# Kernel tuning notes

Measured on AMD Instinct MI355X. Metric: run time of the kernel, lower is better.

## Reference

```python
import jax, jax.numpy as jnp
import numpy as np

POOL_H, POOL_W = 7, 7
SPATIAL_SCALE = 0.25
SAMPLING_RATIO = 2
ALIGNED = True


def setup_inputs() -> dict:
    key = jax.random.key(0)
    k1, k2, k3, k4, k5 = jax.random.split(key, 5)
    N, C, H, W = 4, 256, 200, 200
    K = 1024
    feat = jax.random.normal(k1, (N, C, H, W), dtype=jnp.float32)
    # boxes in image coordinates (image side = H / spatial_scale = 800)
    img = H / SPATIAL_SCALE
    b = jax.random.randint(k2, (K,), 0, N).astype(jnp.float32)
    x1 = jax.random.uniform(k3, (K,)) * (img - 32.0)
    y1 = jax.random.uniform(k4, (K,)) * (img - 32.0)
    wh = jax.random.uniform(k5, (K, 2)) * 256.0 + 16.0
    x2 = jnp.minimum(x1 + wh[:, 0], img - 1.0)
    y2 = jnp.minimum(y1 + wh[:, 1], img - 1.0)
    rois = jnp.stack([b, x1, y1, x2, y2], axis=1)
    return {"input": feat, "rois": rois}


def _roi_align(feat, rois):
    N, C, H, W = feat.shape
    K = rois.shape[0]
    S = SAMPLING_RATIO
    offset = 0.5 if ALIGNED else 0.0

    batch_idx = rois[:, 0].astype(jnp.int32)
    x1 = rois[:, 1] * SPATIAL_SCALE - offset
    y1 = rois[:, 2] * SPATIAL_SCALE - offset
    x2 = rois[:, 3] * SPATIAL_SCALE - offset
    y2 = rois[:, 4] * SPATIAL_SCALE - offset
    roi_w = x2 - x1
    roi_h = y2 - y1
    if not ALIGNED:  # legacy: clamp roi size to at least 1
        roi_w = jnp.maximum(roi_w, 1.0)
        roi_h = jnp.maximum(roi_h, 1.0)
    bin_h = roi_h / POOL_H  # [K]
    bin_w = roi_w / POOL_W

    # sample coordinates: ys [K, PH, S], xs [K, PW, S]
    ph = jnp.arange(POOL_H, dtype=jnp.float32)
    pw = jnp.arange(POOL_W, dtype=jnp.float32)
    s = (jnp.arange(S, dtype=jnp.float32) + 0.5) / S
    ys = y1[:, None, None] + (ph[None, :, None] + s[None, None, :]) * bin_h[:, None, None]
    xs = x1[:, None, None] + (pw[None, :, None] + s[None, None, :]) * bin_w[:, None, None]

    # broadcast to full sample grid [K, PH, S, PW, S]
    y = ys[:, :, :, None, None]
    x = xs[:, None, None, :, :]
    valid = (y > -1.0) & (y < H) & (x > -1.0) & (x < W)

    yc = jnp.clip(y, 0.0, H - 1)
    xc = jnp.clip(x, 0.0, W - 1)
    y0 = jnp.floor(yc).astype(jnp.int32)
    x0 = jnp.floor(xc).astype(jnp.int32)
    y1i = jnp.minimum(y0 + 1, H - 1)
    x1i = jnp.minimum(x0 + 1, W - 1)
    ly = yc - y0
    lx = xc - x0
    hy = 1.0 - ly
    hx = 1.0 - lx

    bi = batch_idx[:, None, None, None, None]
    # advanced indexing -> [K, PH, S, PW, S, C]
    v00 = feat[bi, :, y0, x0]
    v01 = feat[bi, :, y0, x1i]
    v10 = feat[bi, :, y1i, x0]
    v11 = feat[bi, :, y1i, x1i]

    val = ((hy * hx)[..., None] * v00 + (hy * lx)[..., None] * v01
           + (ly * hx)[..., None] * v10 + (ly * lx)[..., None] * v11)
    val = jnp.where(valid[..., None], val, 0.0)

    out = val.sum(axis=(2, 4)) / (S * S)  # [K, PH, PW, C]
    return jnp.transpose(out, (0, 3, 1, 2))  # [K, C, PH, PW]


def reference(input, rois):
    return _roi_align(input, rois)
```

## Files before the change

kernel.cpp:

```cpp
#include <hip/hip_runtime.h>

#define POOL_H 7
#define POOL_W 7
#define BINS   49
#define SR 2
#define SCALE 0.25f
#define CH 256

typedef unsigned int   u32;
typedef unsigned short u16;
typedef unsigned long long u64;
typedef float f2v __attribute__((ext_vector_type(2)));
typedef f2v uf2 __attribute__((aligned(4)));
typedef float f4  __attribute__((ext_vector_type(4)));
typedef u16  us4 __attribute__((ext_vector_type(4)));
typedef u32  ui2 __attribute__((ext_vector_type(2)));
typedef u32  ui4 __attribute__((ext_vector_type(4)));

__device__ __forceinline__ u16 f32_to_bf16_rne(float f) {
    u32 u = __builtin_bit_cast(u32, f);
    u32 r = (u + 0x7FFFu + ((u >> 16) & 1u)) >> 16;
    return (u16)r;
}
__device__ __forceinline__ float bf16lo(u32 u) { return __builtin_bit_cast(float, u << 16); }
__device__ __forceinline__ float bf16hi(u32 u) { return __builtin_bit_cast(float, u & 0xFFFF0000u); }

__global__ __launch_bounds__(512) void nchw_to_nhwc_bf16(
    const float* __restrict__ feat, u16* __restrict__ ft,
    const float* __restrict__ rois, int* __restrict__ perm,
    int HW, int tiles, int K, int H, int W)
{
    __shared__ __align__(16) unsigned char smem[64 * 260 * 2];

    int t = threadIdx.x;

    if ((int)blockIdx.x == gridDim.x - 1) {
        u64* keys = (u64*)smem;
        int bd = (int)blockDim.x;
        for (int v = t; v < 1024; v += bd) {
            u64 kv = ~0ull;
            if (v < K) {
                const float* rp = rois + (size_t)v * 5;
                int b = (int)rp[0];
                float cx = 0.5f * (rp[1] + rp[3]) * SCALE;
                float cy = 0.5f * (rp[2] + rp[4]) * SCALE;
                int qx = min(15, max(0, (int)(cx * (16.0f / (float)W))));
                int qy = min(15, max(0, (int)(cy * (16.0f / (float)H))));
                u32 m = 0;
                #pragma unroll
                for (int i = 0; i < 4; ++i)
                    m |= (((qy >> i) & 1u) << (2 * i + 1)) | (((qx >> i) & 1u) << (2 * i));
                u32 key = ((u32)b << 8) | m;
                kv = ((u64)key << 32) | (u32)v;
            }
            keys[v] = kv;
        }
        __syncthreads();
        for (int size = 2; size <= 1024; size <<= 1) {
            for (int stride = size >> 1; stride > 0; stride >>= 1) {
                for (int v = t; v < 1024; v += bd) {
                    int j = v ^ stride;
                    if (j > v) {
                        bool up = ((v & size) == 0);
                        u64 a = keys[v], bb = keys[j];
                        if ((a > bb) == up) { keys[v] = bb; keys[j] = a; }
                    }
                }
                __syncthreads();
            }
        }
        for (int v = t; v < K; v += bd)
            perm[v] = (int)(keys[v] & 0xffffffffu);
        return;
    }

    u16 (*lds)[260] = (u16 (*)[260])smem;
    int b    = blockIdx.x / tiles;
    int tile = blockIdx.x % tiles;
    int hw0  = tile * 64;

    int lane = t & 63;
    int w    = t >> 6;

    const float* src = feat + (size_t)b * CH * HW + hw0 + lane;
    #pragma unroll 4
    for (int i = 0; i < 32; ++i) {
        int c = w + 8 * i;
        float v = src[(size_t)c * HW];
        lds[lane][c] = f32_to_bf16_rne(v);
    }
    __syncthreads();

    u16* dst = ft + ((size_t)b * HW + hw0) * CH;
    #pragma unroll
    for (int it = 0; it < 4; ++it) {
        int id = it * 512 + t;
        int r  = id >> 5;
        int o  = (id & 31) * 8;
        ui2 lo = __builtin_bit_cast(ui2, *(const us4*)&lds[r][o]);
        ui2 hi = __builtin_bit_cast(ui2, *(const us4*)&lds[r][o + 4]);
        ui4 v = { lo.x, lo.y, hi.x, hi.y };
        *(ui4*)(dst + (size_t)id * 8) = v;
    }
}

__global__ __launch_bounds__(448) void roi_gather_nhwc(
    const u16* __restrict__ ft,
    const float* __restrict__ rois,
    const int* __restrict__ perm,
    float* __restrict__ out,
    int H, int W, int K, int chunk, int do_swz)
{
    int bid  = blockIdx.x;
    int slot = do_swz ? (bid & 7) * chunk + (bid >> 3) : bid;
    int k    = perm[slot / 7];
    int q    = slot % 7;
    int bin0 = q * 7;

    __shared__ float lds[7][CH];

    int lane = threadIdx.x & 63;
    int w    = threadIdx.x >> 6;
    int half = lane >> 5;
    int lc   = lane & 31;

    const float* rp = rois + (size_t)k * 5;
    int   b   = (int)rp[0];
    float rx1 = rp[1] * SCALE - 0.5f;
    float ry1 = rp[2] * SCALE - 0.5f;
    float rx2 = rp[3] * SCALE - 0.5f;
    float ry2 = rp[4] * SCALE - 0.5f;
    float bin_h = (ry2 - ry1) * (1.0f / POOL_H);
    float bin_w = (rx2 - rx1) * (1.0f / POOL_W);

    const u16* fbase = ft + (size_t)b * H * W * CH + lc * 8;

    int ph = q;
    int pw = w;

    float acc[8];
    #pragma unroll
    for (int j = 0; j < 8; ++j) acc[j] = 0.0f;

    #pragma unroll
    for (int iy = 0; iy < SR; ++iy) {
        float y = ry1 + ((float)ph + ((float)iy + 0.5f) * (1.0f / SR)) * bin_h;
        bool vy = (y > -1.0f) && (y < (float)H);
        float yc = fminf(fmaxf(y, 0.0f), (float)(H - 1));
        int   y0 = (int)yc;
        int   y1 = min(y0 + 1, H - 1);
        float ly = yc - (float)y0;
        float hy = 1.0f - ly;
        int   ysel = half ? y1 : y0;
        float wrow = half ? ly : hy;
        #pragma unroll
        for (int ix = 0; ix < SR; ++ix) {
            float x = rx1 + ((float)pw + ((float)ix + 0.5f) * (1.0f / SR)) * bin_w;
            bool vx = (x > -1.0f) && (x < (float)W);
            if (!(vy && vx)) continue;
            float xc = fminf(fmaxf(x, 0.0f), (float)(W - 1));
            int   x0 = (int)xc;
            int   x1 = min(x0 + 1, W - 1);
            float lx = xc - (float)x0;

            const u16* p0 = fbase + (size_t)(ysel * W + x0) * CH;
            ui4 A = *(const ui4*)p0;
            ui4 B = *(const ui4*)(p0 + (size_t)(x1 - x0) * CH);

            #pragma unroll
            for (int j = 0; j < 4; ++j) {
                float a0 = bf16lo(A[j]), a1 = bf16hi(A[j]);
                float b0 = bf16lo(B[j]), b1 = bf16hi(B[j]);
                float r0 = a0 + lx * (b0 - a0);
                float r1 = a1 + lx * (b1 - a1);
                acc[2 * j]     += wrow * r0;
                acc[2 * j + 1] += wrow * r1;
            }
        }
    }

    #pragma unroll
    for (int j = 0; j < 8; ++j)
        acc[j] = (acc[j] + __shfl_xor(acc[j], 32, 64)) * 0.25f;

    if (half == 0) {
        f4 lo = { acc[0], acc[1], acc[2], acc[3] };
        f4 hi = { acc[4], acc[5], acc[6], acc[7] };
        *(f4*)&lds[w][lc * 8]     = lo;
        *(f4*)&lds[w][lc * 8 + 4] = hi;
    }
    __syncthreads();

    float* ob = out + (size_t)k * CH * BINS + bin0;
    for (int id = (int)threadIdx.x; id < 7 * CH; id += 448) {
        int c  = id / 7;
        int lb = id % 7;
        ob[(size_t)c * BINS + lb] = lds[lb][c];
    }
}

#define NC 2
#define NXCD 8
__global__ __launch_bounds__(256) void roi_align_fallback(
    const float* __restrict__ feat, const float* __restrict__ rois,
    float* __restrict__ out, int C, int H, int W, int K,
    int blocks_per_slice, int slices_per_xcd)
{
    int wgid  = blockIdx.x;
    int g     = wgid % NXCD;
    int r     = wgid / NXCD;
    int slice = g * slices_per_xcd + r / blocks_per_slice;
    int j     = r % blocks_per_slice;
    int tid = j * (int)blockDim.x + (int)threadIdx.x;
    int k   = tid / BINS;
    int bin = tid % BINS;
    if (k >= K) return;
    int pw = bin % POOL_W, ph = bin / POOL_W, c2 = slice;

    const float* rp = rois + (size_t)k * 5;
    int b = (int)rp[0];
    float rx1 = rp[1]*SCALE-0.5f, ry1 = rp[2]*SCALE-0.5f;
    float rx2 = rp[3]*SCALE-0.5f, ry2 = rp[4]*SCALE-0.5f;
    float bin_h = (ry2-ry1)*(1.0f/POOL_H), bin_w = (rx2-rx1)*(1.0f/POOL_W);

    int yr0[SR], yr1[SR]; float ly[SR], hy[SR]; bool vy[SR];
    #pragma unroll
    for (int iy = 0; iy < SR; ++iy) {
        float y = ry1 + ((float)ph + ((float)iy+0.5f)*(1.0f/SR))*bin_h;
        vy[iy] = (y > -1.0f) && (y < (float)H);
        float yc = fminf(fmaxf(y, 0.0f), (float)(H-1));
        int y0 = (int)yc; yr0[iy]=y0; yr1[iy]=min(y0+1,H-1);
        ly[iy]=yc-(float)y0; hy[iy]=1.0f-ly[iy];
    }
    int xl[SR]; float lx[SR]; bool vx[SR], xhi[SR];
    #pragma unroll
    for (int ix = 0; ix < SR; ++ix) {
        float x = rx1 + ((float)pw + ((float)ix+0.5f)*(1.0f/SR))*bin_w;
        vx[ix] = (x > -1.0f) && (x < (float)W);
        float xc = fminf(fmaxf(x, 0.0f), (float)(W-1));
        int x0 = (int)xc; int xload = min(x0, W-2);
        xl[ix]=xload; xhi[ix]=(x0>xload); lx[ix]=xc-(float)x0;
    }
    const size_t HW = (size_t)H*W;
    const float* fmap = feat + ((size_t)b*C + (size_t)c2*NC)*HW;
    float acc[NC];
    #pragma unroll
    for (int cc=0; cc<NC; ++cc) acc[cc]=0.0f;
    #pragma unroll
    for (int iy=0; iy<SR; ++iy)
      #pragma unroll
      for (int ix=0; ix<SR; ++ix)
        if (vy[iy] && vx[ix]) {
            int off0 = yr0[iy]*W + xl[ix], off1 = yr1[iy]*W + xl[ix];
            #pragma unroll
            for (int cc=0; cc<NC; ++cc) {
                const float* base = fmap + (size_t)cc*HW;
                f2v d0 = *(const uf2*)(base + off0);
                f2v d1 = *(const uf2*)(base + off1);
                float v00 = xhi[ix] ? d0.y : d0.x;
                float v10 = xhi[ix] ? d1.y : d1.x;
                float r0 = v00 + lx[ix]*(d0.y - v00);
                float r1 = v10 + lx[ix]*(d1.y - v10);
                acc[cc] += hy[iy]*r0 + ly[iy]*r1;
            }
        }
    size_t obase = ((size_t)k*C + (size_t)c2*NC)*BINS + bin;
    #pragma unroll
    for (int cc=0; cc<NC; ++cc)
        out[obase + (size_t)cc*BINS] = acc[cc]*(1.0f/(SR*SR));
}

extern "C" void kernel_launch(void* const* d_in, const int* in_sizes, int n_in,
                              void* d_out, int out_size, void* d_ws, size_t ws_size,
                              hipStream_t stream) {
    const float* feat = (const float*)d_in[0];
    const float* rois = (const float*)d_in[1];
    float* out = (float*)d_out;

    const int C = 256, H = 200, W = 200;
    const int HW = H * W;
    const int K = in_sizes[1] / 5;
    const int N = in_sizes[0] / (C * HW);

    size_t nhwc_bytes = (size_t)N * HW * CH * sizeof(u16);
    size_t need = nhwc_bytes + (size_t)K * sizeof(int);
    if (ws_size >= need && (HW % 64) == 0 && K <= 1024) {
        u16* ft   = (u16*)d_ws;
        int* perm = (int*)((char*)d_ws + nhwc_bytes);
        const int tiles = HW / 64;
        nchw_to_nhwc_bf16<<<N * tiles + 1, 512, 0, stream>>>(
            feat, ft, rois, perm, HW, tiles, K, H, W);
        int grid  = K * 7;
        int swz   = (grid % 8) == 0;
        int chunk = grid / 8;
        roi_gather_nhwc<<<grid, 448, 0, stream>>>(
            (const u16*)ft, rois, perm, out, H, W, K, chunk, swz);
    } else {
        const int threads_per_slice = K * BINS;
        const int block = 256;
        const int blocks_per_slice = (threads_per_slice + block - 1) / block;
        const int slices = C / NC;
        const int slices_per_xcd = slices / NXCD;
        const int grid = slices * blocks_per_slice;
        roi_align_fallback<<<grid, block, 0, stream>>>(feat, rois, out, C, H, W, K,
                                                       blocks_per_slice, slices_per_xcd);
    }
}
```

Before: 92.80 us.

## Widen NCHW-to-NHWC transpose tiles to 128 pixels with packed bf16 pair loads

Measured after the change: 91.86 us. Within noise of the previous version (-1.0%).

```diff
diff --git a/kernel.cpp b/kernel.cpp
--- a/kernel.cpp
+++ b/kernel.cpp
@@ -13,8 +13,6 @@
 typedef float f2v __attribute__((ext_vector_type(2)));
 typedef f2v uf2 __attribute__((aligned(4)));
 typedef float f4  __attribute__((ext_vector_type(4)));
-typedef u16  us4 __attribute__((ext_vector_type(4)));
-typedef u32  ui2 __attribute__((ext_vector_type(2)));
 typedef u32  ui4 __attribute__((ext_vector_type(4)));
 
 __device__ __forceinline__ u16 f32_to_bf16_rne(float f) {
@@ -30,7 +28,7 @@
     const float* __restrict__ rois, int* __restrict__ perm,
     int HW, int tiles, int K, int H, int W)
 {
-    __shared__ __align__(16) unsigned char smem[64 * 260 * 2];
+    extern __shared__ __align__(16) unsigned char smem[];
 
     int t = threadIdx.x;
 
@@ -74,33 +72,58 @@
         return;
     }
 
-    u16 (*lds)[260] = (u16 (*)[260])smem;
+    u32* lds32 = (u32*)smem;
     int b    = blockIdx.x / tiles;
     int tile = blockIdx.x % tiles;
-    int hw0  = tile * 64;
+    int hw0  = tile * 128;
+    int nhw  = min(128, HW - hw0);
 
     int lane = t & 63;
     int w    = t >> 6;
 
-    const float* src = feat + (size_t)b * CH * HW + hw0 + lane;
-    #pragma unroll 4
-    for (int i = 0; i < 32; ++i) {
-        int c = w + 8 * i;
-        float v = src[(size_t)c * HW];
-        lds[lane][c] = f32_to_bf16_rne(v);
+    const float* src = feat + (size_t)b * CH * HW + hw0;
+    if (nhw == 128) {
+        #pragma unroll 8
+        for (int ci = 0; ci < 32; ++ci) {
+            int c = w * 32 + ci;
+            f2v v = *(const f2v*)(src + (size_t)c * HW + 2 * lane);
+            u32 p = ((u32)f32_to_bf16_rne(v.y) << 16) | (u32)f32_to_bf16_rne(v.x);
+            lds32[c * 64 + ((lane + (c >> 3)) & 63)] = p;
+        }
+    } else {
+        #pragma unroll 8
+        for (int ci = 0; ci < 32; ++ci) {
+            int c = w * 32 + ci;
+            float v = src[(size_t)c * HW + lane];
+            u16 h = f32_to_bf16_rne(v);
+            u16* ph = (u16*)&lds32[c * 64 + (((lane >> 1) + (c >> 3)) & 63)];
+            ph[lane & 1] = h;
+        }
     }
     __syncthreads();
 
     u16* dst = ft + ((size_t)b * HW + hw0) * CH;
-    #pragma unroll
-    for (int it = 0; it < 4; ++it) {
-        int id = it * 512 + t;
-        int r  = id >> 5;
-        int o  = (id & 31) * 8;
-        ui2 lo = __builtin_bit_cast(ui2, *(const us4*)&lds[r][o]);
-        ui2 hi = __builtin_bit_cast(ui2, *(const us4*)&lds[r][o + 4]);
-        ui4 v = { lo.x, lo.y, hi.x, hi.y };
-        *(ui4*)(dst + (size_t)id * 8) = v;
+    int cg     = t & 31;
+    int hw_off = t >> 5;
+    int iters  = nhw >> 4;
+    for (int i = 0; i < iters; ++i) {
+        int hw  = i * 16 + hw_off;
+        int m   = hw >> 1;
+        int sel = hw & 1;
+        u32 vals[8];
+        #pragma unroll
+        for (int j = 0; j < 8; ++j) {
+            int c = 8 * cg + j;
+            vals[j] = lds32[c * 64 + ((m + cg) & 63)];
+        }
+        ui4 o;
+        #pragma unroll
+        for (int d = 0; d < 4; ++d) {
+            u32 lo16 = sel ? (vals[2 * d]     >> 16) : (vals[2 * d]     & 0xFFFFu);
+            u32 hi16 = sel ? (vals[2 * d + 1] >> 16) : (vals[2 * d + 1] & 0xFFFFu);
+            o[d] = (hi16 << 16) | lo16;
+        }
+        *(ui4*)(dst + (size_t)hw * CH + cg * 8) = o;
     }
 }
 
@@ -287,8 +310,8 @@
     if (ws_size >= need && (HW % 64) == 0 && K <= 1024) {
         u16* ft   = (u16*)d_ws;
         int* perm = (int*)((char*)d_ws + nhwc_bytes);
-        const int tiles = HW / 64;
-        nchw_to_nhwc_bf16<<<N * tiles + 1, 512, 0, stream>>>(
+        const int tiles = (HW + 127) / 128;
+        nchw_to_nhwc_bf16<<<N * tiles + 1, 512, 65536, stream>>>(
             feat, ft, rois, perm, HW, tiles, K, H, W);
         int grid  = K * 7;
         int swz   = (grid % 8) == 0;
```

## Use direct global-to-LDS loads and split channels across blocks in NHWC transpose

Applied to the files above, without the earlier changes.

New measurement: 96.72 us. 4.2% more time.

```diff
diff --git a/kernel.cpp b/kernel.cpp
--- a/kernel.cpp
+++ b/kernel.cpp
@@ -13,8 +13,6 @@
 typedef float f2v __attribute__((ext_vector_type(2)));
 typedef f2v uf2 __attribute__((aligned(4)));
 typedef float f4  __attribute__((ext_vector_type(4)));
-typedef u16  us4 __attribute__((ext_vector_type(4)));
-typedef u32  ui2 __attribute__((ext_vector_type(2)));
 typedef u32  ui4 __attribute__((ext_vector_type(4)));
 
 __device__ __forceinline__ u16 f32_to_bf16_rne(float f) {
@@ -24,13 +22,20 @@
 }
 __device__ __forceinline__ float bf16lo(u32 u) { return __builtin_bit_cast(float, u << 16); }
 __device__ __forceinline__ float bf16hi(u32 u) { return __builtin_bit_cast(float, u & 0xFFFF0000u); }
+
+__device__ __forceinline__ void gload_lds16(const float* g, float* l) {
+    __builtin_amdgcn_global_load_lds(
+        (const __attribute__((address_space(1))) void*)g,
+        (__attribute__((address_space(3))) void*)l,
+        16, 0, 0);
+}
 
 __global__ __launch_bounds__(512) void nchw_to_nhwc_bf16(
     const float* __restrict__ feat, u16* __restrict__ ft,
     const float* __restrict__ rois, int* __restrict__ perm,
     int HW, int tiles, int K, int H, int W)
 {
-    __shared__ __align__(16) unsigned char smem[64 * 260 * 2];
+    __shared__ __align__(16) unsigned char smem[32768];
 
     int t = threadIdx.x;
 
@@ -74,33 +79,41 @@
         return;
     }
 
-    u16 (*lds)[260] = (u16 (*)[260])smem;
-    int b    = blockIdx.x / tiles;
-    int tile = blockIdx.x % tiles;
-    int hw0  = tile * 64;
+    float* lf = (float*)smem;
+    int bid   = blockIdx.x;
+    int chalf = bid & 1;
+    int tile  = (bid >> 1) % tiles;
+    int b     = (bid >> 1) / tiles;
+    int hw0   = tile * 64;
 
     int lane = t & 63;
     int w    = t >> 6;
 
-    const float* src = feat + (size_t)b * CH * HW + hw0 + lane;
-    #pragma unroll 4
-    for (int i = 0; i < 32; ++i) {
-        int c = w + 8 * i;
-        float v = src[(size_t)c * HW];
-        lds[lane][c] = f32_to_bf16_rne(v);
+    const float* src = feat + ((size_t)b * CH + (size_t)chalf * 128) * HW + hw0;
+    #pragma unroll
+    for (int ii = 0; ii < 4; ++ii) {
+        int i = w * 4 + ii;
+        int r = 4 * i + (lane >> 4);
+        int hwb = (4 * (lane & 15) - 4 * (r >> 3)) & 63;
+        gload_lds16(src + (size_t)r * HW + hwb, &lf[i * 256]);
     }
     __syncthreads();
 
-    u16* dst = ft + ((size_t)b * HW + hw0) * CH;
-    #pragma unroll
-    for (int it = 0; it < 4; ++it) {
-        int id = it * 512 + t;
-        int r  = id >> 5;
-        int o  = (id & 31) * 8;
-        ui2 lo = __builtin_bit_cast(ui2, *(const us4*)&lds[r][o]);
-        ui2 hi = __builtin_bit_cast(ui2, *(const us4*)&lds[r][o + 4]);
-        ui4 v = { lo.x, lo.y, hi.x, hi.y };
-        *(ui4*)(dst + (size_t)id * 8) = v;
+    u16* dst = ft + ((size_t)b * HW + hw0) * CH + chalf * 128;
+    #pragma unroll
+    for (int it = 0; it < 2; ++it) {
+        int cg = t & 15;
+        int hw = it * 32 + (t >> 4);
+        int q  = (hw + 4 * cg) & 63;
+        u32 o[4];
+        #pragma unroll
+        for (int d = 0; d < 4; ++d) {
+            int c0 = 8 * cg + 2 * d;
+            float va = lf[(size_t)c0 * 64 + q];
+            float vb = lf[(size_t)(c0 + 1) * 64 + q];
+            o[d] = ((u32)f32_to_bf16_rne(vb) << 16) | (u32)f32_to_bf16_rne(va);
+        }
+        *(ui4*)(dst + (size_t)hw * CH + 8 * cg) = *(ui4*)o;
     }
 }
 
@@ -288,7 +301,7 @@
         u16* ft   = (u16*)d_ws;
         int* perm = (int*)((char*)d_ws + nhwc_bytes);
         const int tiles = HW / 64;
-        nchw_to_nhwc_bf16<<<N * tiles + 1, 512, 0, stream>>>(
+        nchw_to_nhwc_bf16<<<N * tiles * 2 + 1, 512, 0, stream>>>(
             feat, ft, rois, perm, HW, tiles, K, H, W);
         int grid  = K * 7;
         int swz   = (grid % 8) == 0;
```

## Widen NCHW-to-NHWC bf16 transpose tiles with vector loads and rotated LDS

Applied to the files above, without the earlier changes.

Result: slower. 100.1 us (+7.9%).

```diff
diff --git a/kernel.cpp b/kernel.cpp
--- a/kernel.cpp
+++ b/kernel.cpp
@@ -13,8 +13,6 @@
 typedef float f2v __attribute__((ext_vector_type(2)));
 typedef f2v uf2 __attribute__((aligned(4)));
 typedef float f4  __attribute__((ext_vector_type(4)));
-typedef u16  us4 __attribute__((ext_vector_type(4)));
-typedef u32  ui2 __attribute__((ext_vector_type(2)));
 typedef u32  ui4 __attribute__((ext_vector_type(4)));
 
 __device__ __forceinline__ u16 f32_to_bf16_rne(float f) {
@@ -28,14 +26,13 @@
 __global__ __launch_bounds__(512) void nchw_to_nhwc_bf16(
     const float* __restrict__ feat, u16* __restrict__ ft,
     const float* __restrict__ rois, int* __restrict__ perm,
-    int HW, int tiles, int K, int H, int W)
+    int HW, int nwin, int K, int H, int W, int N)
 {
-    __shared__ __align__(16) unsigned char smem[64 * 260 * 2];
-
+    __shared__ __attribute__((aligned(16))) u32 lds32[32768];
     int t = threadIdx.x;
 
     if ((int)blockIdx.x == gridDim.x - 1) {
-        u64* keys = (u64*)smem;
+        u64* keys = (u64*)lds32;
         int bd = (int)blockDim.x;
         for (int v = t; v < 1024; v += bd) {
             u64 kv = ~0ull;
@@ -74,33 +71,51 @@
         return;
     }
 
-    u16 (*lds)[260] = (u16 (*)[260])smem;
-    int b    = blockIdx.x / tiles;
-    int tile = blockIdx.x % tiles;
-    int hw0  = tile * 64;
+    int bid = blockIdx.x;
+    int b   = bid % N;
+    int win = bid / N;
+    int hw0 = win * 256;
+    int nhw = min(256, HW - hw0);
 
     int lane = t & 63;
     int w    = t >> 6;
 
-    const float* src = feat + (size_t)b * CH * HW + hw0 + lane;
+    const float* src = feat + (size_t)b * CH * HW + hw0 + 4 * lane;
+    bool lok = (4 * lane) < nhw;
+
     #pragma unroll 4
-    for (int i = 0; i < 32; ++i) {
-        int c = w + 8 * i;
-        float v = src[(size_t)c * HW];
-        lds[lane][c] = f32_to_bf16_rne(v);
+    for (int p = 0; p < 16; ++p) {
+        int c2 = w * 16 + p;
+        int c0 = 2 * c2;
+        f4 vA = {0.f,0.f,0.f,0.f}, vB = {0.f,0.f,0.f,0.f};
+        if (lok) {
+            vA = *(const f4*)(src + (size_t)c0 * HW);
+            vB = *(const f4*)(src + (size_t)(c0 + 1) * HW);
+        }
+        ui4 o;
+        o.x = ((u32)f32_to_bf16_rne(vB.x) << 16) | (u32)f32_to_bf16_rne(vA.x);
+        o.y = ((u32)f32_to_bf16_rne(vB.y) << 16) | (u32)f32_to_bf16_rne(vA.y);
+        o.z = ((u32)f32_to_bf16_rne(vB.z) << 16) | (u32)f32_to_bf16_rne(vA.z);
+        o.w = ((u32)f32_to_bf16_rne(vB.w) << 16) | (u32)f32_to_bf16_rne(vA.w);
+        int rot  = c2 & ~3;
+        int word = c2 * 256 + ((4 * lane + rot) & 255);
+        *(ui4*)&lds32[word] = o;
     }
     __syncthreads();
 
     u16* dst = ft + ((size_t)b * HW + hw0) * CH;
-    #pragma unroll
-    for (int it = 0; it < 4; ++it) {
-        int id = it * 512 + t;
-        int r  = id >> 5;
-        int o  = (id & 31) * 8;
-        ui2 lo = __builtin_bit_cast(ui2, *(const us4*)&lds[r][o]);
-        ui2 hi = __builtin_bit_cast(ui2, *(const us4*)&lds[r][o + 4]);
-        ui4 v = { lo.x, lo.y, hi.x, hi.y };
-        *(ui4*)(dst + (size_t)id * 8) = v;
+    int niter = nhw >> 4;
+    for (int i = 0; i < niter; ++i) {
+        int id = i * 512 + t;
+        int hw = id >> 5;
+        int j  = id & 31;
+        u32 o[4];
+        #pragma unroll
+        for (int d = 0; d < 4; ++d) {
+            int c2 = 4 * j + d;
+            o[d] = lds32[c2 * 256 + ((hw + 4 * j) & 255)];
+        }
+        *(ui4*)(dst + (size_t)hw * CH + 8 * j) = *(ui4*)o;
     }
 }
 
@@ -284,12 +299,12 @@
 
     size_t nhwc_bytes = (size_t)N * HW * CH * sizeof(u16);
     size_t need = nhwc_bytes + (size_t)K * sizeof(int);
-    if (ws_size >= need && (HW % 64) == 0 && K <= 1024) {
+    if (ws_size >= need && K <= 1024 && (HW % 64) == 0) {
         u16* ft   = (u16*)d_ws;
         int* perm = (int*)((char*)d_ws + nhwc_bytes);
-        const int tiles = HW / 64;
-        nchw_to_nhwc_bf16<<<N * tiles + 1, 512, 0, stream>>>(
-            feat, ft, rois, perm, HW, tiles, K, H, W);
+        const int nwin = (HW + 255) / 256;
+        nchw_to_nhwc_bf16<<<nwin * N + 1, 512, 0, stream>>>(
+            feat, ft, rois, perm, HW, nwin, K, H, W, N);
         int grid  = K * 7;
         int swz   = (grid % 8) == 0;
         int chunk = grid / 8;
```
